# Kernel optimization log

Measured on AMD Instinct MI355X. Metric: run time of the kernel, lower is better.

The kernel has to match this reference:

```python
import jax, jax.numpy as jnp
import numpy as np

EPS = 1e-8


def setup_inputs() -> dict:
    key = jax.random.key(0)
    k1, k2, k3, k4, k5 = jax.random.split(key, 5)
    N, B, T, D = 8, 2, 2048, 2048
    F = 4 * D
    blocks = jax.random.normal(k1, (N, B, T, D), dtype=jnp.float32)
    partial_block = jax.random.normal(k2, (B, T, D), dtype=jnp.float32)
    proj_w = jax.random.normal(k3, (D,), dtype=jnp.float32) * 0.02
    norm_scale = jnp.ones((D,), dtype=jnp.float32)
    ffn_w1 = jax.random.normal(k4, (D, F), dtype=jnp.float32) * 0.02
    ffn_w2 = jax.random.normal(k5, (F, D), dtype=jnp.float32) * 0.02
    return {
        "blocks": blocks,
        "partial_block": partial_block,
        "proj_w": proj_w,
        "norm_scale": norm_scale,
        "ffn_w1": ffn_w1,
        "ffn_w2": ffn_w2,
    }


def reference(blocks, partial_block, proj_w, norm_scale, ffn_w1, ffn_w2):
    # Stack completed blocks with current partial sum: V [N1, B, T, D]
    V = jnp.concatenate([blocks, partial_block[None]], axis=0)
    # RMSNorm over D (keys)
    rms = jnp.sqrt(jnp.mean(V * V, axis=-1, keepdims=True) + EPS)
    K = norm_scale * V / rms
    # Pseudo-query dot-product logits [N1, B, T], softmax over blocks (axis 0)
    logits = jnp.einsum('nbtd,d->nbt', K, proj_w)
    alpha = jax.nn.softmax(logits, axis=0)
    # Weighted sum of raw values -> new hidden state h [B, T, D]
    h = jnp.einsum('nbt,nbtd->btd', alpha, V)
    # Sublayer: standard FFN (D -> 4D gelu -> D)
    f_out = jax.nn.gelu(h @ ffn_w1) @ ffn_w2
    # layer_number % block_size != 0 branch: accumulate partial sum
    new_partial = partial_block + f_out
    return h, new_partial
```

## Files before the change

kernel.cpp:

```cpp
#include <hip/hip_runtime.h>

typedef unsigned short ushort_t;
typedef __bf16 bf16x8 __attribute__((ext_vector_type(8)));
typedef float f32x4 __attribute__((ext_vector_type(4)));

#define NB 8
#define BB 2
#define TT 2048
#define DD 2048
#define FF 8192
#define MM (BB * TT)
#define BTD ((size_t)BB * TT * DD)

__device__ __forceinline__ unsigned short f2bf(float f) {
  unsigned int u = __float_as_uint(f);
  u += 0x7FFFu + ((u >> 16) & 1u);
  return (unsigned short)(u >> 16);
}

__device__ __forceinline__ float gelu_tanh(float x) {
  float u = 0.7978845608028654f * (x + 0.044715f * x * x * x);
  float e = __expf(2.0f * u);
  float th = 1.0f - 2.0f / (e + 1.0f);
  return 0.5f * x * (1.0f + th);
}

template <int N>
__device__ __forceinline__ void wait_vmcnt() {
  if constexpr (N == 0) asm volatile("s_waitcnt vmcnt(0)" ::: "memory");
  else if constexpr (N == 8) asm volatile("s_waitcnt vmcnt(8)" ::: "memory");
}

#define ASYNC_COPY16(gp, lp)                                                   \
  __builtin_amdgcn_global_load_lds(                                            \
      (__attribute__((address_space(1))) void*)(gp),                           \
      (__attribute__((address_space(3))) void*)(lp), 16, 0, 0)

__global__ __launch_bounds__(256) void transpose_conv(
    const float* __restrict__ in, ushort_t* __restrict__ out, int R, int C) {
  __shared__ float tile[32][33];
  const int tx = threadIdx.x & 31, ty = threadIdx.x >> 5;
  const int r0 = blockIdx.y * 32, c0 = blockIdx.x * 32;
#pragma unroll
  for (int i = 0; i < 32; i += 8)
    tile[ty + i][tx] = in[(size_t)(r0 + ty + i) * C + (c0 + tx)];
  __syncthreads();
#pragma unroll
  for (int i = 0; i < 32; i += 8)
    out[(size_t)(c0 + ty + i) * R + (r0 + tx)] = f2bf(tile[tx][ty + i]);
}

__global__ __launch_bounds__(256) void attn_fuse(
    const float* __restrict__ blocks, const float* __restrict__ partial,
    const float* __restrict__ proj_w, const float* __restrict__ norm_scale,
    float* __restrict__ h_out, ushort_t* __restrict__ h_bf) {
  const int t = threadIdx.x;
  const int bt = blockIdx.x;
  const size_t rowoff = (size_t)bt * DD;
  const int d0 = t * 4;

  float w[8];
  {
    float4 ns = *(const float4*)(norm_scale + d0);
    float4 pw = *(const float4*)(proj_w + d0);
    w[0] = ns.x * pw.x; w[1] = ns.y * pw.y; w[2] = ns.z * pw.z; w[3] = ns.w * pw.w;
    ns = *(const float4*)(norm_scale + 1024 + d0);
    pw = *(const float4*)(proj_w + 1024 + d0);
    w[4] = ns.x * pw.x; w[5] = ns.y * pw.y; w[6] = ns.z * pw.z; w[7] = ns.w * pw.w;
  }

  float vv[9][8];
  float ss[9], dt[9];
#pragma unroll
  for (int n = 0; n < 9; ++n) {
    const float* rp = (n < 8) ? (blocks + (size_t)n * BTD + rowoff)
                              : (partial + rowoff);
    float4 v0 = *(const float4*)(rp + d0);
    float4 v1 = *(const float4*)(rp + 1024 + d0);
    vv[n][0] = v0.x; vv[n][1] = v0.y; vv[n][2] = v0.z; vv[n][3] = v0.w;
    vv[n][4] = v1.x; vv[n][5] = v1.y; vv[n][6] = v1.z; vv[n][7] = v1.w;
    float a = 0.f, c = 0.f;
#pragma unroll
    for (int j = 0; j < 8; ++j) {
      a += vv[n][j] * vv[n][j];
      c += vv[n][j] * w[j];
    }
    ss[n] = a; dt[n] = c;
  }

  __shared__ float red[2][9][4];
  const int lane = t & 63, wv = t >> 6;
#pragma unroll
  for (int n = 0; n < 9; ++n) {
    float a = ss[n], c = dt[n];
#pragma unroll
    for (int off = 32; off > 0; off >>= 1) {
      a += __shfl_down(a, off, 64);
      c += __shfl_down(c, off, 64);
    }
    if (lane == 0) { red[0][n][wv] = a; red[1][n][wv] = c; }
  }
  __syncthreads();
  __shared__ float logit_s[9];
  if (t < 9) {
    float a = red[0][t][0] + red[0][t][1] + red[0][t][2] + red[0][t][3];
    float c = red[1][t][0] + red[1][t][1] + red[1][t][2] + red[1][t][3];
    logit_s[t] = c * rsqrtf(a * (1.0f / (float)DD) + 1e-8f);
  }
  __syncthreads();

  float lg[9], mx = -1e30f;
#pragma unroll
  for (int n = 0; n < 9; ++n) { lg[n] = logit_s[n]; mx = fmaxf(mx, lg[n]); }
  float den = 0.0f;
#pragma unroll
  for (int n = 0; n < 9; ++n) { lg[n] = __expf(lg[n] - mx); den += lg[n]; }
  const float inv = 1.0f / den;

  float h[8] = {0, 0, 0, 0, 0, 0, 0, 0};
#pragma unroll
  for (int n = 0; n < 9; ++n) {
    const float a = lg[n] * inv;
#pragma unroll
    for (int j = 0; j < 8; ++j) h[j] += a * vv[n][j];
  }

  float4 o0 = {h[0], h[1], h[2], h[3]}, o1 = {h[4], h[5], h[6], h[7]};
  *(float4*)(h_out + rowoff + d0) = o0;
  *(float4*)(h_out + rowoff + 1024 + d0) = o1;
  uint2 p0, p1;
  p0.x = (unsigned)f2bf(h[0]) | ((unsigned)f2bf(h[1]) << 16);
  p0.y = (unsigned)f2bf(h[2]) | ((unsigned)f2bf(h[3]) << 16);
  p1.x = (unsigned)f2bf(h[4]) | ((unsigned)f2bf(h[5]) << 16);
  p1.y = (unsigned)f2bf(h[6]) | ((unsigned)f2bf(h[7]) << 16);
  *(uint2*)(h_bf + rowoff + d0) = p0;
  *(uint2*)(h_bf + rowoff + 1024 + d0) = p1;
}

template <int SBY, int SBX, int MCX, int EPI>
__global__ __launch_bounds__(256, 2) void gemm128(
    const ushort_t* __restrict__ A, const ushort_t* __restrict__ BT,
    const int K, const int N, ushort_t* __restrict__ Cb,
    const float* __restrict__ addend, float* __restrict__ Cf) {
  constexpr int AUS = 128 * 64;

  __shared__ __align__(16) ushort_t lds0[2 * AUS];
  __shared__ __align__(16) ushort_t lds1[2 * AUS];

  const int t = threadIdx.x;
  const int lane = t & 63, wv = t >> 6;
  const int wr = (wv >> 1) * 64, wc = (wv & 1) * 64;
  const int fr = lane & 15;

  const int wg = blockIdx.x;
  const int xcd = wg & 7, local = wg >> 3;
  const int sby = local / SBX, sbx = local % SBX;
  const int by = (xcd / MCX) * SBY + sby;
  const int bx = (xcd % MCX) * SBX + sbx;
  const int row0 = by * 128, col0 = bx * 128;

  const int sr = t >> 3;
  const int scolb = ((t & 7) * 16) ^ ((sr & 7) << 4);
  const ushort_t* gA = A + (size_t)(row0 + sr) * K + (scolb >> 1);
  const ushort_t* gB = BT + (size_t)(col0 + sr) * K + (scolb >> 1);

#define ST_A(W, j, KT)                                                         \
  ASYNC_COPY16(gA + (size_t)((j)*32) * K + (KT)*64, &W[(j)*2048 + wv * 512])
#define ST_B(W, j, KT)                                                         \
  ASYNC_COPY16(gB + (size_t)((j)*32) * K + (KT)*64,                            \
               &W[AUS + (j)*2048 + wv * 512])
#define STAGE(W, KT)                                                           \
  {                                                                            \
    ST_A(W, 0, KT); ST_A(W, 1, KT); ST_A(W, 2, KT); ST_A(W, 3, KT);            \
    ST_B(W, 0, KT); ST_B(W, 1, KT); ST_B(W, 2, KT); ST_B(W, 3, KT);            \
  }

  const int s_lane = (fr & 7) << 4;
  const int offk0 = ((lane >> 4) * 16) ^ s_lane;
  const int offk1 = (64 + (lane >> 4) * 16) ^ s_lane;
  const int aoffA = (wr + fr) * 128;
  int boffB[4];
#pragma unroll
  for (int n = 0; n < 4; ++n)
    boffB[n] = AUS * 2 + (wc + n * 16 + fr) * 128;

  f32x4 acc[4][4];
#pragma unroll
  for (int m = 0; m < 4; ++m)
#pragma unroll
    for (int n = 0; n < 4; ++n) {
      f32x4 z = {0.f, 0.f, 0.f, 0.f};
      acc[m][n] = z;
    }

#define MFMA_(a, b, c) __builtin_amdgcn_mfma_f32_16x16x32_bf16(a, b, c, 0, 0, 0)

#define TILE(Rb, KT)                                                           \
  {                                                                            \
    if ((KT) + 1 < NT) wait_vmcnt<8>(); else wait_vmcnt<0>();                  \
    __builtin_amdgcn_s_barrier();                                              \
    const char* _L = (const char*)Rb;                                          \
    bf16x8 af[4][2], bf[4][2];                                                 \
    _Pragma("unroll") for (int m = 0; m < 4; ++m) {                            \
      af[m][0] = *(const bf16x8*)(_L + aoffA + m * 2048 + offk0);              \
      af[m][1] = *(const bf16x8*)(_L + aoffA + m * 2048 + offk1);              \
    }                                                                          \
    _Pragma("unroll") for (int n = 0; n < 4; ++n) {                            \
      bf[n][0] = *(const bf16x8*)(_L + boffB[n] + offk0);                      \
      bf[n][1] = *(const bf16x8*)(_L + boffB[n] + offk1);                      \
    }                                                                          \
    asm volatile("s_waitcnt lgkmcnt(0)" ::: "memory");                         \
    __builtin_amdgcn_s_barrier();             \
    if ((KT) + 2 < NT) STAGE(Rb, (KT) + 2);                                    \
    __builtin_amdgcn_s_setprio(1);                                             \
    _Pragma("unroll") for (int ks = 0; ks < 2; ++ks)                           \
      _Pragma("unroll") for (int m = 0; m < 4; ++m)                            \
        _Pragma("unroll") for (int n = 0; n < 4; ++n)                          \
          acc[m][n] = MFMA_(af[m][ks], bf[n][ks], acc[m][n]);                  \
    __builtin_amdgcn_s_setprio(0);                                             \
  }

  const int NT = K >> 6;

  STAGE(lds0, 0);
  STAGE(lds1, 1);

  for (int kt = 0; kt < NT; kt += 2) {
    TILE(lds0, kt);
    TILE(lds1, kt + 1);
  }

  const int r4 = (lane >> 4) * 4;
#pragma unroll
  for (int m = 0; m < 4; ++m) {
    const int grow = row0 + wr + m * 16 + r4;
#pragma unroll
    for (int n = 0; n < 4; ++n) {
      const int gcol = col0 + wc + n * 16 + fr;
#pragma unroll
      for (int r = 0; r < 4; ++r) {
        const float v = acc[m][n][r];
        const size_t idx = (size_t)(grow + r) * N + gcol;
        if (EPI == 0) {
          Cb[idx] = f2bf(gelu_tanh(v));
        } else {
          Cf[idx] = v + addend[idx];
        }
      }
    }
  }
#undef TILE
#undef MFMA_
#undef STAGE
#undef ST_A
#undef ST_B
}

extern "C" void kernel_launch(void* const* d_in, const int* in_sizes, int n_in,
                              void* d_out, int out_size, void* d_ws,
                              size_t ws_size, hipStream_t stream) {
  const float* blocks = (const float*)d_in[0];
  const float* partial = (const float*)d_in[1];
  const float* proj_w = (const float*)d_in[2];
  const float* norm_scale = (const float*)d_in[3];
  const float* w1 = (const float*)d_in[4];
  const float* w2 = (const float*)d_in[5];

  float* out = (float*)d_out;
  float* h_out = out;
  float* new_partial = out + BTD;

  char* ws = (char*)d_ws;
  ushort_t* h_bf = (ushort_t*)ws;
  ushort_t* w1T = (ushort_t*)(ws + (size_t)16777216);
  ushort_t* w2T = (ushort_t*)(ws + (size_t)16777216 + 33554432);
  ushort_t* act = (ushort_t*)(ws + (size_t)16777216 + 2 * 33554432ull);

  transpose_conv<<<dim3(FF / 32, DD / 32), 256, 0, stream>>>(w1, w1T, DD, FF);
  transpose_conv<<<dim3(DD / 32, FF / 32), 256, 0, stream>>>(w2, w2T, FF, DD);

  attn_fuse<<<MM, 256, 0, stream>>>(blocks, partial, proj_w, norm_scale, h_out,
                                    h_bf);

  gemm128<16, 16, 4, 0><<<(MM / 128) * (FF / 128), 256, 0, stream>>>(
      h_bf, w1T, DD, FF, act, nullptr, nullptr);
  gemm128<8, 8, 2, 1><<<(MM / 128) * (DD / 128), 256, 0, stream>>>(
      act, w2T, FF, DD, nullptr, partial, new_partial);
}
```

Baseline: 393.8 us.

## Replace 128x128 GEMM with 256-row, 512-thread, 4-stage pipelined tile kernel

Replaces the double-buffered 128x128 bf16 GEMM with a templated kernel that uses 256-row tiles, 512 threads (8 waves), a K-step of 32, and a four-deep LDS ring buffer with a three-tile async prefetch. The larger tiles raise operand reuse per global load, and the deeper pipeline hides more load latency. Only one barrier is needed per K-step instead of two. In exchange, LDS use is higher, each block holds more accumulator registers, and with fewer workgroups (512 and 256) the GPU may be less evenly occupied.

```diff
diff --git a/kernel.cpp b/kernel.cpp
--- a/kernel.cpp
+++ b/kernel.cpp
@@ -28,6 +28,9 @@
 template <int N>
 __device__ __forceinline__ void wait_vmcnt() {
   if constexpr (N == 0) asm volatile("s_waitcnt vmcnt(0)" ::: "memory");
+  else if constexpr (N == 3) asm volatile("s_waitcnt vmcnt(3)" ::: "memory");
+  else if constexpr (N == 4) asm volatile("s_waitcnt vmcnt(4)" ::: "memory");
+  else if constexpr (N == 6) asm volatile("s_waitcnt vmcnt(6)" ::: "memory");
   else if constexpr (N == 8) asm volatile("s_waitcnt vmcnt(8)" ::: "memory");
 }
 
@@ -137,106 +140,119 @@
   *(uint2*)(h_bf + rowoff + 1024 + d0) = p1;
 }
 
-template <int SBY, int SBX, int MCX, int EPI>
-__global__ __launch_bounds__(256, 2) void gemm128(
+template <int BN, int WM, int WN, int SBY, int SBX, int MCX, int EPI>
+__global__ __launch_bounds__(512, 2) void gemmQ(
     const ushort_t* __restrict__ A, const ushort_t* __restrict__ BT,
     const int K, const int N, ushort_t* __restrict__ Cb,
     const float* __restrict__ addend, float* __restrict__ Cf) {
-  constexpr int AUS = 128 * 64;
-
-  __shared__ __align__(16) ushort_t lds0[2 * AUS];
-  __shared__ __align__(16) ushort_t lds1[2 * AUS];
+  constexpr int MFR = 256 / WM / 16;
+  constexpr int NFR = BN / WN / 16;
+  constexpr int AS = 16384;
+  constexpr int BS = BN * 64;
+  constexpr int RS = AS + BS;
+  constexpr int LB = BS / 8192;
+  constexpr int LT = 2 + LB;
+
+  __shared__ __align__(16) char lds[4 * RS];
 
   const int t = threadIdx.x;
   const int lane = t & 63, wv = t >> 6;
-  const int wr = (wv >> 1) * 64, wc = (wv & 1) * 64;
-  const int fr = lane & 15;
+  const int fr = lane & 15, kslot = lane >> 4;
+  const int WRow = (wv / WN) * (256 / WM);
+  const int WCol = (wv % WN) * (BN / WN);
 
   const int wg = blockIdx.x;
   const int xcd = wg & 7, local = wg >> 3;
-  const int sby = local / SBX, sbx = local % SBX;
-  const int by = (xcd / MCX) * SBY + sby;
-  const int bx = (xcd % MCX) * SBX + sbx;
-  const int row0 = by * 128, col0 = bx * 128;
-
-  const int sr = t >> 3;
-  const int scolb = ((t & 7) * 16) ^ ((sr & 7) << 4);
-  const ushort_t* gA = A + (size_t)(row0 + sr) * K + (scolb >> 1);
-  const ushort_t* gB = BT + (size_t)(col0 + sr) * K + (scolb >> 1);
-
-#define ST_A(W, j, KT)                                                         \
-  ASYNC_COPY16(gA + (size_t)((j)*32) * K + (KT)*64, &W[(j)*2048 + wv * 512])
-#define ST_B(W, j, KT)                                                         \
-  ASYNC_COPY16(gB + (size_t)((j)*32) * K + (KT)*64,                            \
-               &W[AUS + (j)*2048 + wv * 512])
-#define STAGE(W, KT)                                                           \
+  const int by = (xcd / MCX) * SBY + local / SBX;
+  const int bx = (xcd % MCX) * SBX + local % SBX;
+  const int row0 = by * 256, col0 = bx * BN;
+
+  const ushort_t* ga[2];
+  const ushort_t* gb[LB];
+#pragma unroll
+  for (int j = 0; j < 2; ++j) {
+    const int o = j * 8192 + t * 16;
+    const int rp = o >> 7;
+    const int iX = (o & 127) ^ ((rp & 7) << 4);
+    ga[j] = A + (size_t)(row0 + rp * 2 + (iX >> 6)) * K + ((iX & 63) >> 1);
+  }
+#pragma unroll
+  for (int j = 0; j < LB; ++j) {
+    const int o = j * 8192 + t * 16;
+    const int rp = o >> 7;
+    const int iX = (o & 127) ^ ((rp & 7) << 4);
+    gb[j] = BT + (size_t)(col0 + rp * 2 + (iX >> 6)) * K + ((iX & 63) >> 1);
+  }
+
+#define STAGE(QQ, KT)                                                          \
   {                                                                            \
-    ST_A(W, 0, KT); ST_A(W, 1, KT); ST_A(W, 2, KT); ST_A(W, 3, KT);            \
-    ST_B(W, 0, KT); ST_B(W, 1, KT); ST_B(W, 2, KT); ST_B(W, 3, KT);            \
-  }
-
-  const int s_lane = (fr & 7) << 4;
-  const int offk0 = ((lane >> 4) * 16) ^ s_lane;
-  const int offk1 = (64 + (lane >> 4) * 16) ^ s_lane;
-  const int aoffA = (wr + fr) * 128;
-  int boffB[4];
-#pragma unroll
-  for (int n = 0; n < 4; ++n)
-    boffB[n] = AUS * 2 + (wc + n * 16 + fr) * 128;
-
-  f32x4 acc[4][4];
-#pragma unroll
-  for (int m = 0; m < 4; ++m)
-#pragma unroll
-    for (int n = 0; n < 4; ++n) {
+    ASYNC_COPY16(ga[0] + (size_t)(KT) * 32, lds + (QQ)*RS + t * 16);           \
+    ASYNC_COPY16(ga[1] + (size_t)(KT) * 32, lds + (QQ)*RS + 8192 + t * 16);    \
+    ASYNC_COPY16(gb[0] + (size_t)(KT) * 32, lds + (QQ)*RS + AS + t * 16);      \
+    if constexpr (LB == 2)                                                     \
+      ASYNC_COPY16(gb[1] + (size_t)(KT) * 32,                                  \
+                   lds + (QQ)*RS + AS + 8192 + t * 16);                        \
+  }
+
+  const int arp0 = (WRow + fr) >> 1;
+  const int aoff =
+      arp0 * 128 + (((((fr & 1) << 6) | (kslot << 4))) ^ ((arp0 & 7) << 4));
+  const int brp0 = (WCol + fr) >> 1;
+  const int boff = AS + brp0 * 128 +
+                   (((((fr & 1) << 6) | (kslot << 4))) ^ ((brp0 & 7) << 4));
+
+  f32x4 acc[MFR][NFR];
+#pragma unroll
+  for (int m = 0; m < MFR; ++m)
+#pragma unroll
+    for (int n = 0; n < NFR; ++n) {
       f32x4 z = {0.f, 0.f, 0.f, 0.f};
       acc[m][n] = z;
     }
 
 #define MFMA_(a, b, c) __builtin_amdgcn_mfma_f32_16x16x32_bf16(a, b, c, 0, 0, 0)
 
-#define TILE(Rb, KT)                                                           \
-  {                                                                            \
-    if ((KT) + 1 < NT) wait_vmcnt<8>(); else wait_vmcnt<0>();                  \
-    __builtin_amdgcn_s_barrier();                                              \
-    const char* _L = (const char*)Rb;                                          \
-    bf16x8 af[4][2], bf[4][2];                                                 \
-    _Pragma("unroll") for (int m = 0; m < 4; ++m) {                            \
-      af[m][0] = *(const bf16x8*)(_L + aoffA + m * 2048 + offk0);              \
-      af[m][1] = *(const bf16x8*)(_L + aoffA + m * 2048 + offk1);              \
-    }                                                                          \
-    _Pragma("unroll") for (int n = 0; n < 4; ++n) {                            \
-      bf[n][0] = *(const bf16x8*)(_L + boffB[n] + offk0);                      \
-      bf[n][1] = *(const bf16x8*)(_L + boffB[n] + offk1);                      \
-    }                                                                          \
-    asm volatile("s_waitcnt lgkmcnt(0)" ::: "memory");                         \
-    __builtin_amdgcn_s_barrier();             \
-    if ((KT) + 2 < NT) STAGE(Rb, (KT) + 2);                                    \
-    __builtin_amdgcn_s_setprio(1);                                             \
-    _Pragma("unroll") for (int ks = 0; ks < 2; ++ks)                           \
-      _Pragma("unroll") for (int m = 0; m < 4; ++m)                            \
-        _Pragma("unroll") for (int n = 0; n < 4; ++n)                          \
-          acc[m][n] = MFMA_(af[m][ks], bf[n][ks], acc[m][n]);                  \
-    __builtin_amdgcn_s_setprio(0);                                             \
-  }
-
-  const int NT = K >> 6;
-
-  STAGE(lds0, 0);
-  STAGE(lds1, 1);
-
-  for (int kt = 0; kt < NT; kt += 2) {
-    TILE(lds0, kt);
-    TILE(lds1, kt + 1);
-  }
-
-  const int r4 = (lane >> 4) * 4;
-#pragma unroll
-  for (int m = 0; m < 4; ++m) {
-    const int grow = row0 + wr + m * 16 + r4;
-#pragma unroll
-    for (int n = 0; n < 4; ++n) {
-      const int gcol = col0 + wc + n * 16 + fr;
+  const int NT = K >> 5;
+
+  STAGE(0, 0);
+  STAGE(1, 1);
+  STAGE(2, 2);
+
+  for (int t0 = 0; t0 < NT; t0 += 4) {
+#pragma unroll
+    for (int q = 0; q < 4; ++q) {
+      const int kt = t0 + q;
+      const int rem = NT - 1 - kt;
+      if (rem >= 2) wait_vmcnt<2 * LT>();
+      else if (rem == 1) wait_vmcnt<LT>();
+      else wait_vmcnt<0>();
+      __builtin_amdgcn_s_barrier();
+      if (kt + 3 < NT) STAGE((q + 3) & 3, kt + 3);
+      const char* Lq = lds + q * RS;
+      bf16x8 af[MFR], bfv[NFR];
+#pragma unroll
+      for (int m = 0; m < MFR; ++m)
+        af[m] = *(const bf16x8*)(Lq + aoff + m * 1024);
+#pragma unroll
+      for (int n = 0; n < NFR; ++n)
+        bfv[n] = *(const bf16x8*)(Lq + boff + n * 1024);
+      __builtin_amdgcn_s_setprio(1);
+#pragma unroll
+      for (int m = 0; m < MFR; ++m)
+#pragma unroll
+        for (int n = 0; n < NFR; ++n)
+          acc[m][n] = MFMA_(af[m], bfv[n], acc[m][n]);
+      __builtin_amdgcn_s_setprio(0);
+    }
+  }
+
+  const int r4 = kslot * 4;
+#pragma unroll
+  for (int m = 0; m < MFR; ++m) {
+    const int grow = row0 + WRow + m * 16 + r4;
+#pragma unroll
+    for (int n = 0; n < NFR; ++n) {
+      const int gcol = col0 + WCol + n * 16 + fr;
 #pragma unroll
       for (int r = 0; r < 4; ++r) {
         const float v = acc[m][n][r];
@@ -249,11 +265,8 @@
       }
     }
   }
-#undef TILE
 #undef MFMA_
 #undef STAGE
-#undef ST_A
-#undef ST_B
 }
 
 extern "C" void kernel_launch(void* const* d_in, const int* in_sizes, int n_in,
@@ -282,8 +295,8 @@
   attn_fuse<<<MM, 256, 0, stream>>>(blocks, partial, proj_w, norm_scale, h_out,
                                     h_bf);
 
-  gemm128<16, 16, 4, 0><<<(MM / 128) * (FF / 128), 256, 0, stream>>>(
+  gemmQ<256, 2, 4, 8, 8, 4, 0><<<512, 512, 0, stream>>>(
       h_bf, w1T, DD, FF, act, nullptr, nullptr);
-  gemm128<8, 8, 2, 1><<<(MM / 128) * (DD / 128), 256, 0, stream>>>(
+  gemmQ<128, 4, 2, 4, 8, 2, 1><<<256, 512, 0, stream>>>(
       act, w2T, FF, DD, nullptr, partial, new_partial);
 }
```

Result: no change. 392.7 us (-0.3%).
